# Kernel optimization log

Hardware: AMD Instinct MI355X
Metric: run time of the kernel (lower is better)

## Reference

```python
import jax, jax.numpy as jnp
import numpy as np

N_NODES = 50000


def gcn_conv(x, src, dst, W, b):
    # PyG GCNConv: h = x @ W; out[i] = sum_j norm_ij * h[j] + b, with
    # symmetric normalization over the graph with self-loops (added by caller).
    deg = jax.ops.segment_sum(jnp.ones_like(dst, dtype=x.dtype), dst,
                              num_segments=N_NODES)
    dinv = jnp.where(deg > 0, jax.lax.rsqrt(deg), 0.0)
    norm = dinv[src] * dinv[dst]            # [E+N]
    h = x @ W                                # [N, out]
    msg = h[src] * norm[:, None]             # [E+N, out] gathered messages
    out = jax.ops.segment_sum(msg, dst, num_segments=N_NODES)
    return out + b


def setup_inputs() -> dict:
    key = jax.random.key(0)
    k1, k2, k3, k4, k5 = jax.random.split(key, 5)
    nfeat, nmid, nhid = 128, 128, 128
    x = jax.random.normal(k1, (N_NODES, nfeat), dtype=jnp.float32)
    edge_index = jax.random.randint(k2, (2, 800000), 0, N_NODES, dtype=jnp.int64)
    W1 = jax.random.normal(k3, (nfeat, nmid), dtype=jnp.float32) * 0.05
    b1 = jnp.zeros((nmid,), dtype=jnp.float32)
    W2 = jax.random.normal(k4, (nmid, nhid), dtype=jnp.float32) * 0.05
    b2 = jnp.zeros((nhid,), dtype=jnp.float32)
    return {"x": x, "edge_index": edge_index, "W1": W1, "b1": b1,
            "W2": W2, "b2": b2}


def reference(x, edge_index, W1, b1, W2, b2):
    # add self-loops once; both GCNConv layers use the same graph
    loops = jnp.arange(N_NODES, dtype=edge_index.dtype)
    src = jnp.concatenate([edge_index[0], loops])
    dst = jnp.concatenate([edge_index[1], loops])
    h = jax.nn.relu(gcn_conv(x, src, dst, W1, b1))
    h = jax.nn.relu(gcn_conv(h, src, dst, W2, b2))
    return h
```

## Files before the change

### kernel.cpp

```cpp
#include <hip/hip_runtime.h>
#include <hip/hip_fp16.h>

#define N_NODES 50000
#define F 128
#define RANGE 12500
#define LDK 136
#define PAD 64
#define GEMMB 391
#define CNTB 2048

typedef _Float16 f16x8 __attribute__((ext_vector_type(8)));
typedef float    f32x4 __attribute__((ext_vector_type(4)));

__global__ void k_prep(int* __restrict__ cnt,
                       const float* __restrict__ W1, const float* __restrict__ W2,
                       __half* __restrict__ Wt1, __half* __restrict__ Wt2) {
    const int b = blockIdx.x;
    if (b < 196) {
        const int i = b * 256 + threadIdx.x;
        if (i < N_NODES) cnt[i] = 0;
    } else {
        const float* W  = (b == 196) ? W1 : W2;
        __half*      Wt = (b == 196) ? Wt1 : Wt2;
        for (int i = threadIdx.x; i < F * F; i += 256) {
            const int k = i >> 7, n = i & 127;
            Wt[n * F + k] = __float2half(W[i]);
        }
    }
}

__device__ inline void gemm_tile(const float* __restrict__ X,
                                 const __half* __restrict__ Wt,
                                 const float* __restrict__ dinv,
                                 __half* __restrict__ Hs, int nrows, int r0,
                                 __half* Xs, __half* Ws) {
    const int t    = threadIdx.x;
    const int wid  = t >> 6;
    const int lane = t & 63;

    {
        const uint4* Wg = (const uint4*)Wt;
        const int n = t >> 2, c0 = (t & 3) * 4;
        uint4* drow = (uint4*)&Ws[n * LDK];
#pragma unroll
        for (int j = 0; j < 4; ++j) drow[c0 + j] = Wg[n * 16 + c0 + j];
    }
    {
        const int xr = t >> 2, c0 = (t & 3) * 32;
        const int grow = min(r0 + xr, nrows - 1);
        const float4* Xg = (const float4*)(X + (size_t)grow * F);
        __half2* xd = (__half2*)&Xs[xr * LDK + c0];
#pragma unroll
        for (int j = 0; j < 8; ++j) {
            const float4 v = Xg[c0 / 4 + j];
            xd[2 * j]     = __float22half2_rn(make_float2(v.x, v.y));
            xd[2 * j + 1] = __float22half2_rn(make_float2(v.z, v.w));
        }
    }
    __syncthreads();

    const int m  = lane & 15;
    const int kg = lane >> 4;
    f32x4 acc[8] = {};
#pragma unroll
    for (int kk = 0; kk < 4; ++kk) {
        const f16x8 a = *(const f16x8*)&Xs[(wid * 16 + m) * LDK + kk * 32 + kg * 8];
#pragma unroll
        for (int nt = 0; nt < 8; ++nt) {
            const f16x8 bfr = *(const f16x8*)&Ws[(nt * 16 + m) * LDK + kk * 32 + kg * 8];
            acc[nt] = __builtin_amdgcn_mfma_f32_16x16x32_f16(a, bfr, acc[nt], 0, 0, 0);
        }
    }
    __syncthreads();

    {
        const int lr0 = wid * 16 + kg * 4;
#pragma unroll
        for (int r = 0; r < 4; ++r) {
            const int lr = lr0 + r;
            const float dn = dinv ? dinv[min(r0 + lr, nrows - 1)] : 1.0f;
#pragma unroll
            for (int nt = 0; nt < 8; ++nt)
                Xs[lr * LDK + nt * 16 + m] = __float2half(dn * acc[nt][r]);
        }
    }
    __syncthreads();
    {
        const int row = t >> 2, c0 = (t & 3) * 4;
        const int g = r0 + row;
        if (g < nrows) {
            const uint4* srow = (const uint4*)&Xs[row * LDK];
            uint4* drow = (uint4*)(Hs + (size_t)g * F);
#pragma unroll
            for (int j = 0; j < 4; ++j) drow[c0 + j] = srow[c0 + j];
        }
    }
}

__global__ __launch_bounds__(512) void k_cg1(const float* __restrict__ X,
                                             const __half* __restrict__ Wt1,
                                             __half* __restrict__ Hs,
                                             const int* __restrict__ src,
                                             const int* __restrict__ dst, int E,
                                             int* __restrict__ cnt,
                                             unsigned short* __restrict__ csrP) {
    __shared__ __half Xs[128 * LDK];
    __shared__ __half Ws[128 * LDK];
    if (blockIdx.x < GEMMB) {
        gemm_tile(X, Wt1, nullptr, Hs, N_NODES, blockIdx.x * 128, Xs, Ws);
    } else {
        const int bid = blockIdx.x - GEMMB;
        const int r  = bid & 3;
        const int lo = r * RANGE, hi = min(lo + RANGE, N_NODES);
        const int base   = (bid >> 2) * 512 + threadIdx.x;
        const int stride = (CNTB >> 2) * 512;
        for (int i = base; i < E; i += stride) {
            const int d = dst[i];
            const int s = src[i];
            if (d >= lo && d < hi) {
                const int pos = atomicAdd(&cnt[d], 1);
                if (pos < PAD) csrP[d * PAD + pos] = (unsigned short)s;
            }
        }
    }
}

__global__ __launch_bounds__(512) void k_sdv(const int* __restrict__ cnt,
                                             float* __restrict__ dinv,
                                             __half* __restrict__ Hs) {
    const int tid = blockIdx.x * 512 + threadIdx.x;
    const int nth = gridDim.x * 512;
    for (int n = tid; n < N_NODES; n += nth)
        dinv[n] = rsqrtf((float)(cnt[n] + 1));
    uint4* __restrict__ Hv = (uint4*)Hs;
    const int total = N_NODES * 16;
    for (int i = tid; i < total; i += nth) {
        const float dn = rsqrtf((float)(cnt[i >> 4] + 1));
        uint4 v = Hv[i];
        __half2* h = (__half2*)&v;
#pragma unroll
        for (int j = 0; j < 4; ++j) {
            float2 f = __half22float2(h[j]);
            h[j] = __float22half2_rn(make_float2(dn * f.x, dn * f.y));
        }
        Hv[i] = v;
    }
}

__global__ __launch_bounds__(512) void k_gemm(const float* __restrict__ X,
                                              const __half* __restrict__ Wt,
                                              const float* __restrict__ dinv,
                                              __half* __restrict__ Hs, int nrows) {
    __shared__ __half Xs[128 * LDK];
    __shared__ __half Ws[128 * LDK];
    gemm_tile(X, Wt, dinv, Hs, nrows, blockIdx.x * 128, Xs, Ws);
}

__global__ __launch_bounds__(256) void k_gather(const int* __restrict__ cnt,
                                                const unsigned short* __restrict__ csrP,
                                                const __half* __restrict__ Hs,
                                                const float* __restrict__ dinv,
                                                const float* __restrict__ b,
                                                float* __restrict__ out) {
    const int tid = blockIdx.x * blockDim.x + threadIdx.x;
    const int g   = tid >> 5;
    const int l32 = threadIdx.x & 31;
    const int ng  = (gridDim.x * blockDim.x) >> 5;
    const uint2* __restrict__ Hv = (const uint2*)Hs;
    float4* __restrict__ outv = (float4*)out;
    const float4 bb = ((const float4*)b)[l32];
    for (int n = g; n < N_NODES; n += ng) {
        const int beg = n * PAD;
        const int end = beg + min(cnt[n], PAD);
        float4 a0 = make_float4(0.f, 0.f, 0.f, 0.f);
        float4 a1 = make_float4(0.f, 0.f, 0.f, 0.f);
        float4 a2 = make_float4(0.f, 0.f, 0.f, 0.f);
        float4 a3 = make_float4(0.f, 0.f, 0.f, 0.f);
        {
            const uint2 raw = Hv[n * 32 + l32];
            const float2 f0 = __half22float2(*(const __half2*)&raw.x);
            const float2 f1 = __half22float2(*(const __half2*)&raw.y);
            a0.x += f0.x; a0.y += f0.y; a0.z += f1.x; a0.w += f1.y;
        }
        int e = beg;
        for (; e + 3 < end; e += 4) {
            const int s0 = csrP[e];
            const int s1 = csrP[e + 1];
            const int s2 = csrP[e + 2];
            const int s3 = csrP[e + 3];
            const uint2 r0 = Hv[s0 * 32 + l32];
            const uint2 r1 = Hv[s1 * 32 + l32];
            const uint2 r2 = Hv[s2 * 32 + l32];
            const uint2 r3 = Hv[s3 * 32 + l32];
            float2 f;
            f = __half22float2(*(const __half2*)&r0.x); a0.x += f.x; a0.y += f.y;
            f = __half22float2(*(const __half2*)&r0.y); a0.z += f.x; a0.w += f.y;
            f = __half22float2(*(const __half2*)&r1.x); a1.x += f.x; a1.y += f.y;
            f = __half22float2(*(const __half2*)&r1.y); a1.z += f.x; a1.w += f.y;
            f = __half22float2(*(const __half2*)&r2.x); a2.x += f.x; a2.y += f.y;
            f = __half22float2(*(const __half2*)&r2.y); a2.z += f.x; a2.w += f.y;
            f = __half22float2(*(const __half2*)&r3.x); a3.x += f.x; a3.y += f.y;
            f = __half22float2(*(const __half2*)&r3.y); a3.z += f.x; a3.w += f.y;
        }
        for (; e < end; ++e) {
            const uint2 r0 = Hv[csrP[e] * 32 + l32];
            float2 f;
            f = __half22float2(*(const __half2*)&r0.x); a1.x += f.x; a1.y += f.y;
            f = __half22float2(*(const __half2*)&r0.y); a1.z += f.x; a1.w += f.y;
        }
        const float dn = dinv[n];
        float4 o;
        o.x = fmaxf(fmaf(dn, (a0.x + a1.x) + (a2.x + a3.x), bb.x), 0.f);
        o.y = fmaxf(fmaf(dn, (a0.y + a1.y) + (a2.y + a3.y), bb.y), 0.f);
        o.z = fmaxf(fmaf(dn, (a0.z + a1.z) + (a2.z + a3.z), bb.z), 0.f);
        o.w = fmaxf(fmaf(dn, (a0.w + a1.w) + (a2.w + a3.w), bb.w), 0.f);
        outv[n * 32 + l32] = o;
    }
}

extern "C" void kernel_launch(void* const* d_in, const int* in_sizes, int n_in,
                              void* d_out, int out_size, void* d_ws, size_t ws_size,
                              hipStream_t stream) {
    const float* x  = (const float*)d_in[0];
    const int*   ei = (const int*)  d_in[1];
    const float* W1 = (const float*)d_in[2];
    const float* b1 = (const float*)d_in[3];
    const float* W2 = (const float*)d_in[4];
    const float* b2 = (const float*)d_in[5];
    float* out = (float*)d_out;

    const int E = in_sizes[1] / 2;
    const int* srcp = ei;
    const int* dstp = ei + E;

    int*            cnt  = (int*)d_ws;
    float*          dinv = (float*)(cnt + N_NODES);
    unsigned short* csrP = (unsigned short*)(dinv + N_NODES);
    __half*         Hs   = (__half*)(csrP + (size_t)N_NODES * PAD);
    __half*         Wt1  = Hs + (size_t)N_NODES * F;
    __half*         Wt2  = Wt1 + F * F;

    k_prep  <<<198, 256, 0, stream>>>(cnt, W1, W2, Wt1, Wt2);
    k_cg1   <<<GEMMB + CNTB, 512, 0, stream>>>(x, Wt1, Hs, srcp, dstp, E, cnt, csrP);
    k_sdv   <<<256, 512, 0, stream>>>(cnt, dinv, Hs);
    k_gather<<<2048, 256, 0, stream>>>(cnt, csrP, Hs, dinv, b1, out);
    k_gemm  <<<GEMMB, 512, 0, stream>>>(out, Wt2, dinv, Hs, N_NODES);
    k_gather<<<2048, 256, 0, stream>>>(cnt, csrP, Hs, dinv, b2, out);
}
```

Baseline: 152.8 us.

## Split H into four 32-column feature slices to shrink the gather working set

The GEMM epilogue now writes the fp16 hidden matrix as four column-slice planes of 32 features each, and the scaling kernel is adjusted to index that layout. The gather kernel walks the slices one after another with 16-lane groups, so each pass only touches a 3.2 MB slice of H that is more likely to stay in cache. In exchange, the CSR index list and counts are re-read four times, each gathered row becomes a 64-byte access instead of 256 bytes, and output writes become strided float2 stores.

```diff
diff --git a/kernel.cpp b/kernel.cpp
--- a/kernel.cpp
+++ b/kernel.cpp
@@ -11,6 +11,7 @@
 
 typedef _Float16 f16x8 __attribute__((ext_vector_type(8)));
 typedef float    f32x4 __attribute__((ext_vector_type(4)));
+
 
 __global__ void k_prep(int* __restrict__ cnt,
                        const float* __restrict__ W1, const float* __restrict__ W2,
@@ -86,13 +87,13 @@
     }
     __syncthreads();
     {
-        const int row = t >> 2, c0 = (t & 3) * 4;
+        const int row = t >> 2, sl = t & 3;
         const int g = r0 + row;
         if (g < nrows) {
-            const uint4* srow = (const uint4*)&Xs[row * LDK];
-            uint4* drow = (uint4*)(Hs + (size_t)g * F);
-#pragma unroll
-            for (int j = 0; j < 4; ++j) drow[c0 + j] = srow[c0 + j];
+            const uint4* srow = (const uint4*)&Xs[row * LDK + sl * 32];
+            uint4* drow = (uint4*)(Hs + ((size_t)sl * N_NODES + g) * 32);
+#pragma unroll
+            for (int j = 0; j < 4; ++j) drow[j] = srow[j];
         }
     }
 }
@@ -133,9 +134,10 @@
     for (int n = tid; n < N_NODES; n += nth)
         dinv[n] = rsqrtf((float)(cnt[n] + 1));
     uint4* __restrict__ Hv = (uint4*)Hs;
-    const int total = N_NODES * 16;
+    const int total = 4 * N_NODES * 4;
     for (int i = tid; i < total; i += nth) {
-        const float dn = rsqrtf((float)(cnt[i >> 4] + 1));
+        const int node = (i >> 2) % N_NODES;
+        const float dn = rsqrtf((float)(cnt[node] + 1));
         uint4 v = Hv[i];
         __half2* h = (__half2*)&v;
 #pragma unroll
@@ -162,59 +164,52 @@
                                                 const float* __restrict__ dinv,
                                                 const float* __restrict__ b,
                                                 float* __restrict__ out) {
-    const int tid = blockIdx.x * blockDim.x + threadIdx.x;
-    const int g   = tid >> 5;
-    const int l32 = threadIdx.x & 31;
-    const int ng  = (gridDim.x * blockDim.x) >> 5;
-    const uint2* __restrict__ Hv = (const uint2*)Hs;
-    float4* __restrict__ outv = (float4*)out;
-    const float4 bb = ((const float4*)b)[l32];
-    for (int n = g; n < N_NODES; n += ng) {
-        const int beg = n * PAD;
-        const int end = beg + min(cnt[n], PAD);
-        float4 a0 = make_float4(0.f, 0.f, 0.f, 0.f);
-        float4 a1 = make_float4(0.f, 0.f, 0.f, 0.f);
-        float4 a2 = make_float4(0.f, 0.f, 0.f, 0.f);
-        float4 a3 = make_float4(0.f, 0.f, 0.f, 0.f);
-        {
-            const uint2 raw = Hv[n * 32 + l32];
-            const float2 f0 = __half22float2(*(const __half2*)&raw.x);
-            const float2 f1 = __half22float2(*(const __half2*)&raw.y);
-            a0.x += f0.x; a0.y += f0.y; a0.z += f1.x; a0.w += f1.y;
-        }
-        int e = beg;
-        for (; e + 3 < end; e += 4) {
-            const int s0 = csrP[e];
-            const int s1 = csrP[e + 1];
-            const int s2 = csrP[e + 2];
-            const int s3 = csrP[e + 3];
-            const uint2 r0 = Hv[s0 * 32 + l32];
-            const uint2 r1 = Hv[s1 * 32 + l32];
-            const uint2 r2 = Hv[s2 * 32 + l32];
-            const uint2 r3 = Hv[s3 * 32 + l32];
-            float2 f;
-            f = __half22float2(*(const __half2*)&r0.x); a0.x += f.x; a0.y += f.y;
-            f = __half22float2(*(const __half2*)&r0.y); a0.z += f.x; a0.w += f.y;
-            f = __half22float2(*(const __half2*)&r1.x); a1.x += f.x; a1.y += f.y;
-            f = __half22float2(*(const __half2*)&r1.y); a1.z += f.x; a1.w += f.y;
-            f = __half22float2(*(const __half2*)&r2.x); a2.x += f.x; a2.y += f.y;
-            f = __half22float2(*(const __half2*)&r2.y); a2.z += f.x; a2.w += f.y;
-            f = __half22float2(*(const __half2*)&r3.x); a3.x += f.x; a3.y += f.y;
-            f = __half22float2(*(const __half2*)&r3.y); a3.z += f.x; a3.w += f.y;
-        }
-        for (; e < end; ++e) {
-            const uint2 r0 = Hv[csrP[e] * 32 + l32];
-            float2 f;
-            f = __half22float2(*(const __half2*)&r0.x); a1.x += f.x; a1.y += f.y;
-            f = __half22float2(*(const __half2*)&r0.y); a1.z += f.x; a1.w += f.y;
-        }
-        const float dn = dinv[n];
-        float4 o;
-        o.x = fmaxf(fmaf(dn, (a0.x + a1.x) + (a2.x + a3.x), bb.x), 0.f);
-        o.y = fmaxf(fmaf(dn, (a0.y + a1.y) + (a2.y + a3.y), bb.y), 0.f);
-        o.z = fmaxf(fmaf(dn, (a0.z + a1.z) + (a2.z + a3.z), bb.z), 0.f);
-        o.w = fmaxf(fmaf(dn, (a0.w + a1.w) + (a2.w + a3.w), bb.w), 0.f);
-        outv[n * 32 + l32] = o;
+    const int tid = blockIdx.x * 256 + threadIdx.x;
+    const int g   = tid >> 4;
+    const int l16 = threadIdx.x & 15;
+    const int ng  = (gridDim.x * 256) >> 4;
+#pragma unroll
+    for (int sl = 0; sl < 4; ++sl) {
+        const uint* __restrict__ Hv = (const uint*)(Hs + (size_t)sl * N_NODES * 32);
+        const float2 bb = *(const float2*)&b[sl * 32 + l16 * 2];
+        for (int n = g; n < N_NODES; n += ng) {
+            const int beg = n * PAD;
+            const int end = beg + min(cnt[n], PAD);
+            float2 a0, a1, a2, a3;
+            {
+                const uint raw = Hv[n * 16 + l16];
+                a0 = __half22float2(*(const __half2*)&raw);
+            }
+            a1 = make_float2(0.f, 0.f);
+            a2 = make_float2(0.f, 0.f);
+            a3 = make_float2(0.f, 0.f);
+            int e = beg;
+            for (; e + 3 < end; e += 4) {
+                const int s0 = csrP[e];
+                const int s1 = csrP[e + 1];
+                const int s2 = csrP[e + 2];
+                const int s3 = csrP[e + 3];
+                const uint r0 = Hv[s0 * 16 + l16];
+                const uint r1 = Hv[s1 * 16 + l16];
+                const uint r2 = Hv[s2 * 16 + l16];
+                const uint r3 = Hv[s3 * 16 + l16];
+                float2 f;
+                f = __half22float2(*(const __half2*)&r0); a0.x += f.x; a0.y += f.y;
+                f = __half22float2(*(const __half2*)&r1); a1.x += f.x; a1.y += f.y;
+                f = __half22float2(*(const __half2*)&r2); a2.x += f.x; a2.y += f.y;
+                f = __half22float2(*(const __half2*)&r3); a3.x += f.x; a3.y += f.y;
+            }
+            for (; e < end; ++e) {
+                const uint r0 = Hv[csrP[e] * 16 + l16];
+                float2 f = __half22float2(*(const __half2*)&r0);
+                a1.x += f.x; a1.y += f.y;
+            }
+            const float dn = dinv[n];
+            float2 o;
+            o.x = fmaxf(fmaf(dn, (a0.x + a1.x) + (a2.x + a3.x), bb.x), 0.f);
+            o.y = fmaxf(fmaf(dn, (a0.y + a1.y) + (a2.y + a3.y), bb.y), 0.f);
+            *(float2*)&out[(size_t)n * F + sl * 32 + l16 * 2] = o;
+        }
     }
 }
 
```

Measured after the change: 193.3 us. 26.5% more time.

## Remove source-scaling pass by folding degree normalization into layer-1 gather

Applied to the files above, without the earlier changes.

Drops the separate kernel that computed dinv and rescaled the whole fp16 H buffer in place. The layer-1 gather now applies the source-side normalization per edge by reading cnt[src] and taking rsqrt, and the layer-2 GEMM computes rsqrt(cnt+1) directly instead of reading a dinv array. This removes one launch plus a full read-modify-write of H (about 12.8 MB), in exchange for an extra scattered 4-byte cnt load and an rsqrt per edge in the first gather.

```diff
diff --git a/kernel.cpp b/kernel.cpp
--- a/kernel.cpp
+++ b/kernel.cpp
@@ -31,7 +31,7 @@
 
 __device__ inline void gemm_tile(const float* __restrict__ X,
                                  const __half* __restrict__ Wt,
-                                 const float* __restrict__ dinv,
+                                 const int* __restrict__ cnt,
                                  __half* __restrict__ Hs, int nrows, int r0,
                                  __half* Xs, __half* Ws) {
     const int t    = threadIdx.x;
@@ -78,7 +78,8 @@
 #pragma unroll
         for (int r = 0; r < 4; ++r) {
             const int lr = lr0 + r;
-            const float dn = dinv ? dinv[min(r0 + lr, nrows - 1)] : 1.0f;
+            const float dn = cnt ? rsqrtf((float)(cnt[min(r0 + lr, nrows - 1)] + 1))
+                                 : 1.0f;
 #pragma unroll
             for (int nt = 0; nt < 8; ++nt)
                 Xs[lr * LDK + nt * 16 + m] = __float2half(dn * acc[nt][r]);
@@ -125,41 +126,19 @@
     }
 }
 
-__global__ __launch_bounds__(512) void k_sdv(const int* __restrict__ cnt,
-                                             float* __restrict__ dinv,
-                                             __half* __restrict__ Hs) {
-    const int tid = blockIdx.x * 512 + threadIdx.x;
-    const int nth = gridDim.x * 512;
-    for (int n = tid; n < N_NODES; n += nth)
-        dinv[n] = rsqrtf((float)(cnt[n] + 1));
-    uint4* __restrict__ Hv = (uint4*)Hs;
-    const int total = N_NODES * 16;
-    for (int i = tid; i < total; i += nth) {
-        const float dn = rsqrtf((float)(cnt[i >> 4] + 1));
-        uint4 v = Hv[i];
-        __half2* h = (__half2*)&v;
-#pragma unroll
-        for (int j = 0; j < 4; ++j) {
-            float2 f = __half22float2(h[j]);
-            h[j] = __float22half2_rn(make_float2(dn * f.x, dn * f.y));
-        }
-        Hv[i] = v;
-    }
-}
-
 __global__ __launch_bounds__(512) void k_gemm(const float* __restrict__ X,
                                               const __half* __restrict__ Wt,
-                                              const float* __restrict__ dinv,
+                                              const int* __restrict__ cnt,
                                               __half* __restrict__ Hs, int nrows) {
     __shared__ __half Xs[128 * LDK];
     __shared__ __half Ws[128 * LDK];
-    gemm_tile(X, Wt, dinv, Hs, nrows, blockIdx.x * 128, Xs, Ws);
-}
-
+    gemm_tile(X, Wt, cnt, Hs, nrows, blockIdx.x * 128, Xs, Ws);
+}
+
+template <bool SCALE_SRC>
 __global__ __launch_bounds__(256) void k_gather(const int* __restrict__ cnt,
                                                 const unsigned short* __restrict__ csrP,
                                                 const __half* __restrict__ Hs,
-                                                const float* __restrict__ dinv,
                                                 const float* __restrict__ b,
                                                 float* __restrict__ out) {
     const int tid = blockIdx.x * blockDim.x + threadIdx.x;
@@ -170,17 +149,20 @@
     float4* __restrict__ outv = (float4*)out;
     const float4 bb = ((const float4*)b)[l32];
     for (int n = g; n < N_NODES; n += ng) {
+        const int cn  = cnt[n];
+        const float dn = rsqrtf((float)(cn + 1));
         const int beg = n * PAD;
-        const int end = beg + min(cnt[n], PAD);
+        const int end = beg + min(cn, PAD);
         float4 a0 = make_float4(0.f, 0.f, 0.f, 0.f);
         float4 a1 = make_float4(0.f, 0.f, 0.f, 0.f);
         float4 a2 = make_float4(0.f, 0.f, 0.f, 0.f);
         float4 a3 = make_float4(0.f, 0.f, 0.f, 0.f);
         {
+            const float ds = SCALE_SRC ? dn : 1.0f;
             const uint2 raw = Hv[n * 32 + l32];
             const float2 f0 = __half22float2(*(const __half2*)&raw.x);
             const float2 f1 = __half22float2(*(const __half2*)&raw.y);
-            a0.x += f0.x; a0.y += f0.y; a0.z += f1.x; a0.w += f1.y;
+            a0.x = ds * f0.x; a0.y = ds * f0.y; a0.z = ds * f1.x; a0.w = ds * f1.y;
         }
         int e = beg;
         for (; e + 3 < end; e += 4) {
@@ -188,27 +170,45 @@
             const int s1 = csrP[e + 1];
             const int s2 = csrP[e + 2];
             const int s3 = csrP[e + 3];
+            float ds0 = 1.f, ds1 = 1.f, ds2 = 1.f, ds3 = 1.f;
+            if (SCALE_SRC) {
+                ds0 = rsqrtf((float)(cnt[s0] + 1));
+                ds1 = rsqrtf((float)(cnt[s1] + 1));
+                ds2 = rsqrtf((float)(cnt[s2] + 1));
+                ds3 = rsqrtf((float)(cnt[s3] + 1));
+            }
             const uint2 r0 = Hv[s0 * 32 + l32];
             const uint2 r1 = Hv[s1 * 32 + l32];
             const uint2 r2 = Hv[s2 * 32 + l32];
             const uint2 r3 = Hv[s3 * 32 + l32];
             float2 f;
-            f = __half22float2(*(const __half2*)&r0.x); a0.x += f.x; a0.y += f.y;
-            f = __half22float2(*(const __half2*)&r0.y); a0.z += f.x; a0.w += f.y;
-            f = __half22float2(*(const __half2*)&r1.x); a1.x += f.x; a1.y += f.y;
-            f = __half22float2(*(const __half2*)&r1.y); a1.z += f.x; a1.w += f.y;
-            f = __half22float2(*(const __half2*)&r2.x); a2.x += f.x; a2.y += f.y;
-            f = __half22float2(*(const __half2*)&r2.y); a2.z += f.x; a2.w += f.y;
-            f = __half22float2(*(const __half2*)&r3.x); a3.x += f.x; a3.y += f.y;
-            f = __half22float2(*(const __half2*)&r3.y); a3.z += f.x; a3.w += f.y;
+            f = __half22float2(*(const __half2*)&r0.x);
+            a0.x = fmaf(ds0, f.x, a0.x); a0.y = fmaf(ds0, f.y, a0.y);
+            f = __half22float2(*(const __half2*)&r0.y);
+            a0.z = fmaf(ds0, f.x, a0.z); a0.w = fmaf(ds0, f.y, a0.w);
+            f = __half22float2(*(const __half2*)&r1.x);
+            a1.x = fmaf(ds1, f.x, a1.x); a1.y = fmaf(ds1, f.y, a1.y);
+            f = __half22float2(*(const __half2*)&r1.y);
+            a1.z = fmaf(ds1, f.x, a1.z); a1.w = fmaf(ds1, f.y, a1.w);
+            f = __half22float2(*(const __half2*)&r2.x);
+            a2.x = fmaf(ds2, f.x, a2.x); a2.y = fmaf(ds2, f.y, a2.y);
+            f = __half22float2(*(const __half2*)&r2.y);
+            a2.z = fmaf(ds2, f.x, a2.z); a2.w = fmaf(ds2, f.y, a2.w);
+            f = __half22float2(*(const __half2*)&r3.x);
+            a3.x = fmaf(ds3, f.x, a3.x); a3.y = fmaf(ds3, f.y, a3.y);
+            f = __half22float2(*(const __half2*)&r3.y);
+            a3.z = fmaf(ds3, f.x, a3.z); a3.w = fmaf(ds3, f.y, a3.w);
         }
         for (; e < end; ++e) {
-            const uint2 r0 = Hv[csrP[e] * 32 + l32];
+            const int s0 = csrP[e];
+            const float ds0 = SCALE_SRC ? rsqrtf((float)(cnt[s0] + 1)) : 1.0f;
+            const uint2 r0 = Hv[s0 * 32 + l32];
             float2 f;
-            f = __half22float2(*(const __half2*)&r0.x); a1.x += f.x; a1.y += f.y;
-            f = __half22float2(*(const __half2*)&r0.y); a1.z += f.x; a1.w += f.y;
-        }
-        const float dn = dinv[n];
+            f = __half22float2(*(const __half2*)&r0.x);
+            a0.x = fmaf(ds0, f.x, a0.x); a0.y = fmaf(ds0, f.y, a0.y);
+            f = __half22float2(*(const __half2*)&r0.y);
+            a0.z = fmaf(ds0, f.x, a0.z); a0.w = fmaf(ds0, f.y, a0.w);
+        }
         float4 o;
         o.x = fmaxf(fmaf(dn, (a0.x + a1.x) + (a2.x + a3.x), bb.x), 0.f);
         o.y = fmaxf(fmaf(dn, (a0.y + a1.y) + (a2.y + a3.y), bb.y), 0.f);
@@ -234,16 +234,15 @@
     const int* dstp = ei + E;
 
     int*            cnt  = (int*)d_ws;
-    float*          dinv = (float*)(cnt + N_NODES);
-    unsigned short* csrP = (unsigned short*)(dinv + N_NODES);
+    unsigned short* csrP = (unsigned short*)(cnt + N_NODES);
     __half*         Hs   = (__half*)(csrP + (size_t)N_NODES * PAD);
     __half*         Wt1  = Hs + (size_t)N_NODES * F;
     __half*         Wt2  = Wt1 + F * F;
 
-    k_prep  <<<198, 256, 0, stream>>>(cnt, W1, W2, Wt1, Wt2);
-    k_cg1   <<<GEMMB + CNTB, 512, 0, stream>>>(x, Wt1, Hs, srcp, dstp, E, cnt, csrP);
-    k_sdv   <<<256, 512, 0, stream>>>(cnt, dinv, Hs);
-    k_gather<<<2048, 256, 0, stream>>>(cnt, csrP, Hs, dinv, b1, out);
-    k_gemm  <<<GEMMB, 512, 0, stream>>>(out, Wt2, dinv, Hs, N_NODES);
-    k_gather<<<2048, 256, 0, stream>>>(cnt, csrP, Hs, dinv, b2, out);
-}
+    k_prep         <<<198, 256, 0, stream>>>(cnt, W1, W2, Wt1, Wt2);
+    k_cg1          <<<GEMMB + CNTB, 512, 0, stream>>>(x, Wt1, Hs, srcp, dstp, E,
+                                                      cnt, csrP);
+    k_gather<true> <<<2048, 256, 0, stream>>>(cnt, csrP, Hs, b1, out);
+    k_gemm         <<<GEMMB, 512, 0, stream>>>(out, Wt2, cnt, Hs, N_NODES);
+    k_gather<false><<<2048, 256, 0, stream>>>(cnt, csrP, Hs, b2, out);
+}
```

Result: slower. 161.3 us (+5.6%).
